# Optimization experiments

Hardware: AMD Instinct MI355X
Metric: run time of the kernel (lower is better)

## Reference

```python
import jax, jax.numpy as jnp
import numpy as np


def _squash(t, axis):
    # matches torch: t / norm * (norm^2 / (1 + norm^2))
    ns = jnp.sum(t * t, axis=axis, keepdims=True)
    norm = jnp.sqrt(ns)
    return t / norm * (ns / (1.0 + ns))


def setup_inputs() -> dict:
    key = jax.random.key(0)
    k1, k2 = jax.random.split(key)
    B, I, A_IN, O, A_OUT = 16, 2048, 16, 64, 32
    x = jax.random.normal(k1, (B, I, A_IN, 1), dtype=jnp.float32)
    # nn.init.normal(std=0.1)
    weights = jax.random.normal(k2, (I, A_IN, O * A_OUT), dtype=jnp.float32) * 0.1
    # nn.init.constant(val=0.1)
    bias = jnp.full((O, A_OUT), 0.1, dtype=jnp.float32)
    return {"x": x, "weights": weights, "bias": bias}


def reference(x, weights, bias):
    B = x.shape[0]
    I, A_IN, OA = weights.shape
    O, A = bias.shape
    NUM_ROUTING = 3  # hardcoded in the torch forward

    # votes = sum over input_atoms of broadcast(x) * weights  -> [B, I, O, A]
    votes = jnp.einsum('bia,iaj->bij', x[..., 0], weights).reshape(B, I, O, A)
    votes_sg = jax.lax.stop_gradient(votes)

    logits = jnp.zeros((B, I, O), dtype=votes.dtype)
    activation = None
    for i in range(NUM_ROUTING):
        route = jax.nn.softmax(logits, axis=2)  # over output_dim
        v = votes if i == NUM_ROUTING - 1 else votes_sg
        # weighted sum over input capsules: [B, O, A]
        preactivate = jnp.einsum('bio,bioa->boa', route, v) + bias
        activation = _squash(preactivate, axis=2)
        if i < NUM_ROUTING - 1:
            # agreement between votes and current output capsules
            distances = jnp.einsum('bioa,boa->bio', votes, activation)
            logits = logits + distances
    return activation
```

## Files before the change

kernel.cpp:

```cpp
#include <hip/hip_runtime.h>
#include <hip/hip_fp16.h>
#include <math.h>

#define B_   16
#define I_   2048
#define AIN_ 16
#define O_   64
#define J_   2048
#define JP_  1024

__device__ __forceinline__ float2 ntload2(const float2* p) {
  union { double d; float2 f; } u;
  u.d = __builtin_nontemporal_load((const double*)p);
  return u.f;
}

__device__ __forceinline__ void unp8(const uint4 u, float2* f) {
  const __half2* h = (const __half2*)&u;
  f[0] = __half22float2(h[0]); f[1] = __half22float2(h[1]);
  f[2] = __half22float2(h[2]); f[3] = __half22float2(h[3]);
}
__device__ __forceinline__ uint4 pk8(float4 a, float4 b) {
  union { uint4 u; __half2 h[4]; } r;
  r.h[0] = __float22half2_rn(make_float2(a.x, a.y));
  r.h[1] = __float22half2_rn(make_float2(a.z, a.w));
  r.h[2] = __float22half2_rn(make_float2(b.x, b.y));
  r.h[3] = __float22half2_rn(make_float2(b.z, b.w));
  return r.u;
}

__global__ __launch_bounds__(256) void votes_p0_kernel(
    const float* __restrict__ x, const float* __restrict__ W,
    __half2* __restrict__ votes, __half2* __restrict__ part0)
{
  __shared__ __half2 x_lds[4][B_][AIN_];
  const int tid = threadIdx.x;
  const int islab = blockIdx.x >> 2, jt = blockIdx.x & 3;
  const int i0 = islab * 4;

  for (int e = tid; e < 4 * B_ * AIN_; e += 256) {
    int il = e >> 8, b = (e >> 4) & 15, a = e & 15;
    float xv = x[((size_t)b * I_ + (i0 + il)) * AIN_ + a];
    x_lds[il][b][a] = __float2half2_rn(xv);
  }
  __syncthreads();

  const int jp = jt * 256 + tid;
  __half2 acc[16];
  #pragma unroll
  for (int b = 0; b < 16; ++b) acc[b] = __float2half2_rn(0.f);

  for (int il = 0; il < 4; ++il) {
    const int i = i0 + il;
    const float2* __restrict__ Wi =
        (const float2*)W + (size_t)i * (AIN_ * JP_) + jp;

    __half2 v[16];
    #pragma unroll
    for (int b = 0; b < 16; ++b) v[b] = __float2half2_rn(0.f);

    #pragma unroll
    for (int a2 = 0; a2 < 8; ++a2) {
      __half2 w0 = __float22half2_rn(ntload2(Wi + (size_t)(2 * a2 + 0) * JP_));
      __half2 w1 = __float22half2_rn(ntload2(Wi + (size_t)(2 * a2 + 1) * JP_));
      #pragma unroll
      for (int b = 0; b < 16; ++b) {
        v[b] = __hfma2(x_lds[il][b][2 * a2],     w0, v[b]);
        v[b] = __hfma2(x_lds[il][b][2 * a2 + 1], w1, v[b]);
      }
    }

    __half2* __restrict__ vo = votes + (size_t)i * (B_ * JP_) + jp;
    #pragma unroll
    for (int b = 0; b < 16; ++b) {
      vo[(size_t)b * JP_] = v[b];
      acc[b] = __hadd2(acc[b], v[b]);
    }
  }

  const __half2 s64 = __float2half2_rn(1.0f / 64.0f);
  __half2* __restrict__ po = part0 + (size_t)blockIdx.x * (B_ * 256) + tid;
  #pragma unroll
  for (int b = 0; b < 16; ++b)
    po[(size_t)b * 256] = __hmul2(acc[b], s64);
}

__global__ __launch_bounds__(256) void reduce_squash0_f16(
    const uint4* __restrict__ part0, const float* __restrict__ bias,
    float* __restrict__ act)
{
  __shared__ float red[64][4][8];
  const int b = blockIdx.x >> 6, o = blockIdx.x & 63;
  const int t = threadIdx.x, s = t >> 2, q = t & 3;
  const uint4* __restrict__ base =
      part0 + (size_t)(o >> 4) * 1024 + b * 64 + (o & 15) * 4 + q;

  float r[8];
  #pragma unroll
  for (int e = 0; e < 8; ++e) r[e] = 0.f;
  #pragma unroll
  for (int k = 0; k < 8; ++k) {
    uint4 u = base[(size_t)(s + 64 * k) * 4096];
    float2 f[4];
    unp8(u, f);
    r[0] += f[0].x; r[1] += f[0].y; r[2] += f[1].x; r[3] += f[1].y;
    r[4] += f[2].x; r[5] += f[2].y; r[6] += f[3].x; r[7] += f[3].y;
  }
  #pragma unroll
  for (int e = 0; e < 8; ++e) red[s][q][e] = r[e];
  __syncthreads();

  if (t < 32) {
    const int q2 = t >> 3, e = t & 7;
    float p = 0.f;
    for (int s2 = 0; s2 < 64; ++s2) p += red[s2][q2][e];
    p += bias[o * 32 + q2 * 8 + e];
    float ns = p * p;
    ns += __shfl_xor(ns, 1);  ns += __shfl_xor(ns, 2);
    ns += __shfl_xor(ns, 4);  ns += __shfl_xor(ns, 8);
    ns += __shfl_xor(ns, 16);
    act[(size_t)b * J_ + o * 32 + q2 * 8 + e] = p * sqrtf(ns) / (1.0f + ns);
  }
}

template<int PASS>
__global__ __launch_bounds__(256) void route_kernel(
    const uint4* __restrict__ votes4, const float* __restrict__ act_in,
    uint4* __restrict__ part, float* __restrict__ logits)
{
  __shared__ float d_lds[128];
  __shared__ float r_lds[128];

  const int t = threadIdx.x;
  const int islab = blockIdx.x >> 3, bq = blockIdx.x & 7;
  const int i0 = islab * 8;
  const int o = t >> 2, l4 = t & 3;
  const float4* __restrict__ actq = (const float4*)act_in;

  float4 av00 = actq[(size_t)(bq * 2 + 0) * 512 + 2 * t];
  float4 av01 = actq[(size_t)(bq * 2 + 0) * 512 + 2 * t + 1];
  float4 av10 = actq[(size_t)(bq * 2 + 1) * 512 + 2 * t];
  float4 av11 = actq[(size_t)(bq * 2 + 1) * 512 + 2 * t + 1];

  float4 ac00 = make_float4(0,0,0,0), ac01 = make_float4(0,0,0,0);
  float4 ac10 = make_float4(0,0,0,0), ac11 = make_float4(0,0,0,0);

  for (int il = 0; il < 8; ++il) {
    const int i = i0 + il;
    float lgv = 0.f;
    if (PASS == 2 && t < 128)
      lgv = logits[((size_t)(bq * 2 + (t >> 6)) * I_ + i) * O_ + (t & 63)];

    const uint4* __restrict__ vo =
        votes4 + (size_t)i * 4096 + (size_t)(bq * 2) * 256 + t;
    float2 f0[4], f1[4];
    unp8(vo[0],   f0);
    unp8(vo[256], f1);

    float c0 = f0[0].x*av00.x + f0[0].y*av00.y + f0[1].x*av00.z + f0[1].y*av00.w
             + f0[2].x*av01.x + f0[2].y*av01.y + f0[3].x*av01.z + f0[3].y*av01.w;
    c0 += __shfl_xor(c0, 1);  c0 += __shfl_xor(c0, 2);
    float c1 = f1[0].x*av10.x + f1[0].y*av10.y + f1[1].x*av10.z + f1[1].y*av10.w
             + f1[2].x*av11.x + f1[2].y*av11.y + f1[3].x*av11.z + f1[3].y*av11.w;
    c1 += __shfl_xor(c1, 1);  c1 += __shfl_xor(c1, 2);
    if (l4 == 0) d_lds[o]      = c0;
    if (l4 == 1) d_lds[64 + o] = c1;
    __syncthreads();

    float ellsave = 0.f;
    if (t < 128) {
      float ell = d_lds[t];
      if (PASS == 2) ell += lgv;
      ellsave = ell;
      float m = ell;
      m = fmaxf(m, __shfl_xor(m, 32)); m = fmaxf(m, __shfl_xor(m, 16));
      m = fmaxf(m, __shfl_xor(m, 8));  m = fmaxf(m, __shfl_xor(m, 4));
      m = fmaxf(m, __shfl_xor(m, 2));  m = fmaxf(m, __shfl_xor(m, 1));
      float e = __expf(ell - m);
      float sd = e;
      sd += __shfl_xor(sd, 32); sd += __shfl_xor(sd, 16); sd += __shfl_xor(sd, 8);
      sd += __shfl_xor(sd, 4);  sd += __shfl_xor(sd, 2);  sd += __shfl_xor(sd, 1);
      r_lds[t] = e / sd;
    }
    __syncthreads();

    if (PASS == 1 && t < 128)
      logits[((size_t)(bq * 2 + (t >> 6)) * I_ + i) * O_ + (t & 63)] = ellsave;

    float r0 = r_lds[o], r1 = r_lds[64 + o];
    ac00.x = fmaf(r0, f0[0].x, ac00.x); ac00.y = fmaf(r0, f0[0].y, ac00.y);
    ac00.z = fmaf(r0, f0[1].x, ac00.z); ac00.w = fmaf(r0, f0[1].y, ac00.w);
    ac01.x = fmaf(r0, f0[2].x, ac01.x); ac01.y = fmaf(r0, f0[2].y, ac01.y);
    ac01.z = fmaf(r0, f0[3].x, ac01.z); ac01.w = fmaf(r0, f0[3].y, ac01.w);
    ac10.x = fmaf(r1, f1[0].x, ac10.x); ac10.y = fmaf(r1, f1[0].y, ac10.y);
    ac10.z = fmaf(r1, f1[1].x, ac10.z); ac10.w = fmaf(r1, f1[1].y, ac10.w);
    ac11.x = fmaf(r1, f1[2].x, ac11.x); ac11.y = fmaf(r1, f1[2].y, ac11.y);
    ac11.z = fmaf(r1, f1[3].x, ac11.z); ac11.w = fmaf(r1, f1[3].y, ac11.w);
  }

  uint4* __restrict__ po =
      part + (size_t)islab * 4096 + (size_t)(bq * 2) * 256 + t;
  po[0]   = pk8(ac00, ac01);
  po[256] = pk8(ac10, ac11);
}

__global__ __launch_bounds__(256) void reduce_squash_f16(
    const uint4* __restrict__ part, const float* __restrict__ bias,
    float* __restrict__ out)
{
  __shared__ float red[64][4][8];
  const int b = blockIdx.x >> 6, o = blockIdx.x & 63;
  const int t = threadIdx.x, s = t >> 2, q = t & 3;
  const uint4* __restrict__ base =
      part + (size_t)b * 256 + o * 4 + q;

  float r[8];
  #pragma unroll
  for (int e = 0; e < 8; ++e) r[e] = 0.f;
  #pragma unroll
  for (int k = 0; k < 4; ++k) {
    uint4 u = base[(size_t)(s + 64 * k) * 4096];
    float2 f[4];
    unp8(u, f);
    r[0] += f[0].x; r[1] += f[0].y; r[2] += f[1].x; r[3] += f[1].y;
    r[4] += f[2].x; r[5] += f[2].y; r[6] += f[3].x; r[7] += f[3].y;
  }
  #pragma unroll
  for (int e = 0; e < 8; ++e) red[s][q][e] = r[e];
  __syncthreads();

  if (t < 32) {
    const int q2 = t >> 3, e = t & 7;
    float p = 0.f;
    for (int s2 = 0; s2 < 64; ++s2) p += red[s2][q2][e];
    p += bias[o * 32 + q2 * 8 + e];
    float ns = p * p;
    ns += __shfl_xor(ns, 1);  ns += __shfl_xor(ns, 2);
    ns += __shfl_xor(ns, 4);  ns += __shfl_xor(ns, 8);
    ns += __shfl_xor(ns, 16);
    out[(size_t)b * J_ + o * 32 + q2 * 8 + e] = p * sqrtf(ns) / (1.0f + ns);
  }
}

__global__ __launch_bounds__(256) void reduce_squash_f32(
    const float* __restrict__ part, const float* __restrict__ bias,
    float* __restrict__ out)
{
  __shared__ float4 red[32][8];
  const int b = blockIdx.x >> 6, o = blockIdx.x & 63;
  const int t = threadIdx.x, s = t >> 3, q = t & 7;
  const float4* __restrict__ base =
      (const float4*)part + (size_t)b * 512 + o * 8 + q;

  float4 acc = make_float4(0.f, 0.f, 0.f, 0.f);
  #pragma unroll
  for (int k = 0; k < 8; ++k) {
    float4 v = base[(size_t)(s + 32 * k) * 8192];
    acc.x += v.x; acc.y += v.y; acc.z += v.z; acc.w += v.w;
  }
  red[s][q] = acc;
  __syncthreads();

  if (t < 8) {
    float4 p = make_float4(0.f, 0.f, 0.f, 0.f);
    for (int s2 = 0; s2 < 32; ++s2) {
      float4 v = red[s2][t];
      p.x += v.x; p.y += v.y; p.z += v.z; p.w += v.w;
    }
    float4 bq4 = ((const float4*)bias)[o * 8 + t];
    p.x += bq4.x; p.y += bq4.y; p.z += bq4.z; p.w += bq4.w;
    float ns = p.x*p.x + p.y*p.y + p.z*p.z + p.w*p.w;
    ns += __shfl_xor(ns, 1);  ns += __shfl_xor(ns, 2);  ns += __shfl_xor(ns, 4);
    float sc = sqrtf(ns) / (1.0f + ns);
    ((float4*)out)[(size_t)b * 512 + o * 8 + t] =
        make_float4(p.x*sc, p.y*sc, p.z*sc, p.w*sc);
  }
}

template<int PASS>
__global__ __launch_bounds__(1024) void fb_pass_kernel(
    const float* __restrict__ x, const float* __restrict__ W,
    const float* __restrict__ act_in, float* __restrict__ part,
    float* __restrict__ logits)
{
  __shared__ float x_lds[8 * B_ * AIN_];
  __shared__ float d_lds[8 * O_];
  __shared__ float r_lds[8 * O_];
  const int tid = threadIdx.x, blk = blockIdx.x, i0 = blk * 8;
  for (int e = tid; e < 8 * B_ * AIN_; e += 1024) {
    int b = e >> 7, il = (e >> 4) & 7, a = e & 15;
    x_lds[il * 256 + b * 16 + a] =
        x[(size_t)b * (I_ * AIN_) + (size_t)(i0 + il) * AIN_ + a];
  }
  __syncthreads();
  const int og = tid >> 4, lg = tid & 15;
  float2 acc[16];
  #pragma unroll
  for (int b = 0; b < 16; ++b) acc[b] = make_float2(0.f, 0.f);
  const float2* __restrict__ Wq   = (const float2*)W;
  const float2* __restrict__ actq = (const float2*)act_in;
  for (int il = 0; il < 8; ++il) {
    const int i = i0 + il;
    const float2* __restrict__ Wi = Wq + (size_t)i * (AIN_ * JP_);
    const float4* __restrict__ xq = (const float4*)x_lds + il * 64;
    for (int h = 0; h < 2; ++h) {
      float2 v[8];
      #pragma unroll
      for (int bb = 0; bb < 8; ++bb) v[bb] = make_float2(0.f, 0.f);
      #pragma unroll
      for (int a4 = 0; a4 < 4; ++a4) {
        float2 w0 = Wi[(size_t)(a4 * 4 + 0) * JP_ + tid];
        float2 w1 = Wi[(size_t)(a4 * 4 + 1) * JP_ + tid];
        float2 w2 = Wi[(size_t)(a4 * 4 + 2) * JP_ + tid];
        float2 w3 = Wi[(size_t)(a4 * 4 + 3) * JP_ + tid];
        #pragma unroll
        for (int bb = 0; bb < 8; ++bb) {
          float4 xv = xq[(h * 8 + bb) * 4 + a4];
          v[bb].x = fmaf(xv.x, w0.x, v[bb].x); v[bb].y = fmaf(xv.x, w0.y, v[bb].y);
          v[bb].x = fmaf(xv.y, w1.x, v[bb].x); v[bb].y = fmaf(xv.y, w1.y, v[bb].y);
          v[bb].x = fmaf(xv.z, w2.x, v[bb].x); v[bb].y = fmaf(xv.z, w2.y, v[bb].y);
          v[bb].x = fmaf(xv.w, w3.x, v[bb].x); v[bb].y = fmaf(xv.w, w3.y, v[bb].y);
        }
      }
      if (PASS == 0) {
        #pragma unroll
        for (int bb = 0; bb < 8; ++bb) {
          acc[h * 8 + bb].x += v[bb].x; acc[h * 8 + bb].y += v[bb].y;
        }
      } else {
        #pragma unroll
        for (int bb = 0; bb < 8; ++bb) {
          const int b = h * 8 + bb;
          float2 avv = actq[(size_t)b * JP_ + tid];
          float c = v[bb].x * avv.x + v[bb].y * avv.y;
          c += __shfl_xor(c, 1); c += __shfl_xor(c, 2);
          c += __shfl_xor(c, 4); c += __shfl_xor(c, 8);
          if (lg == bb) d_lds[bb * 64 + og] = c;
        }
        __syncthreads();
        if (tid < 512) {
          const int bb2 = tid >> 6, o2 = tid & 63;
          const int b2  = h * 8 + bb2;
          float ell = d_lds[tid];
          if (PASS == 2) ell += logits[((size_t)b2 * I_ + i) * O_ + o2];
          if (PASS == 1) logits[((size_t)b2 * I_ + i) * O_ + o2] = ell;
          float m = ell;
          m = fmaxf(m, __shfl_xor(m, 32)); m = fmaxf(m, __shfl_xor(m, 16));
          m = fmaxf(m, __shfl_xor(m, 8));  m = fmaxf(m, __shfl_xor(m, 4));
          m = fmaxf(m, __shfl_xor(m, 2));  m = fmaxf(m, __shfl_xor(m, 1));
          float e = __expf(ell - m);
          float s = e;
          s += __shfl_xor(s, 32); s += __shfl_xor(s, 16); s += __shfl_xor(s, 8);
          s += __shfl_xor(s, 4);  s += __shfl_xor(s, 2);  s += __shfl_xor(s, 1);
          r_lds[tid] = e / s;
        }
        __syncthreads();
        #pragma unroll
        for (int bb = 0; bb < 8; ++bb) {
          float r = r_lds[bb * 64 + og];
          acc[h * 8 + bb].x = fmaf(r, v[bb].x, acc[h * 8 + bb].x);
          acc[h * 8 + bb].y = fmaf(r, v[bb].y, acc[h * 8 + bb].y);
        }
      }
    }
  }
  const float sc = (PASS == 0) ? (1.0f / 64.0f) : 1.0f;
  #pragma unroll
  for (int b = 0; b < 16; ++b) {
    float2* __restrict__ po = (float2*)part +
        (size_t)blk * (B_ * JP_) + (size_t)b * JP_ + tid;
    *po = make_float2(acc[b].x * sc, acc[b].y * sc);
  }
}

extern "C" void kernel_launch(void* const* d_in, const int* in_sizes, int n_in,
                              void* d_out, int out_size, void* d_ws, size_t ws_size,
                              hipStream_t stream) {
  const float* x    = (const float*)d_in[0];
  const float* W    = (const float*)d_in[1];
  const float* bias = (const float*)d_in[2];
  float* out = (float*)d_out;

  float*   part   = (float*)d_ws;
  float*   act    = part + (size_t)256 * (B_ * J_);
  float*   logits = act + (B_ * J_);
  __half2* votes  = (__half2*)(logits + (size_t)B_ * I_ * O_);
  const size_t need = ((size_t)256 * B_ * J_ + B_ * J_ + (size_t)B_ * I_ * O_) * 4
                    + (size_t)I_ * B_ * JP_ * 4;

  if (ws_size >= need) {
    votes_p0_kernel<<<2048, 256, 0, stream>>>(x, W, votes, (__half2*)part);
    reduce_squash0_f16<<<1024, 256, 0, stream>>>((const uint4*)part, bias, act);
    route_kernel<1><<<2048, 256, 0, stream>>>((const uint4*)votes, act,
                                              (uint4*)part, logits);
    reduce_squash_f16<<<1024, 256, 0, stream>>>((const uint4*)part, bias, act);
    route_kernel<2><<<2048, 256, 0, stream>>>((const uint4*)votes, act,
                                              (uint4*)part, logits);
    reduce_squash_f16<<<1024, 256, 0, stream>>>((const uint4*)part, bias, out);
  } else {
    fb_pass_kernel<0><<<256, 1024, 0, stream>>>(x, W, act, part, logits);
    reduce_squash_f32<<<1024, 256, 0, stream>>>(part, bias, act);
    fb_pass_kernel<1><<<256, 1024, 0, stream>>>(x, W, act, part, logits);
    reduce_squash_f32<<<1024, 256, 0, stream>>>(part, bias, act);
    fb_pass_kernel<2><<<256, 1024, 0, stream>>>(x, W, act, part, logits);
    reduce_squash_f32<<<1024, 256, 0, stream>>>(part, bias, out);
  }
}
```

Baseline: 164.6 us.

## Batch routing softmax across eight inputs to cut per-iteration block barriers

```diff
diff --git a/kernel.cpp b/kernel.cpp
--- a/kernel.cpp
+++ b/kernel.cpp
@@ -128,50 +128,51 @@
     const uint4* __restrict__ votes4, const float* __restrict__ act_in,
     uint4* __restrict__ part, float* __restrict__ logits)
 {
-  __shared__ float d_lds[128];
-  __shared__ float r_lds[128];
+  __shared__ float d_lds[8][128];
+  __shared__ float r_lds[8][128];
 
   const int t = threadIdx.x;
   const int islab = blockIdx.x >> 3, bq = blockIdx.x & 7;
   const int i0 = islab * 8;
   const int o = t >> 2, l4 = t & 3;
   const float4* __restrict__ actq = (const float4*)act_in;
-
-  float4 av00 = actq[(size_t)(bq * 2 + 0) * 512 + 2 * t];
-  float4 av01 = actq[(size_t)(bq * 2 + 0) * 512 + 2 * t + 1];
-  float4 av10 = actq[(size_t)(bq * 2 + 1) * 512 + 2 * t];
-  float4 av11 = actq[(size_t)(bq * 2 + 1) * 512 + 2 * t + 1];
-
-  float4 ac00 = make_float4(0,0,0,0), ac01 = make_float4(0,0,0,0);
-  float4 ac10 = make_float4(0,0,0,0), ac11 = make_float4(0,0,0,0);
-
-  for (int il = 0; il < 8; ++il) {
-    const int i = i0 + il;
-    float lgv = 0.f;
-    if (PASS == 2 && t < 128)
-      lgv = logits[((size_t)(bq * 2 + (t >> 6)) * I_ + i) * O_ + (t & 63)];
-
-    const uint4* __restrict__ vo =
-        votes4 + (size_t)i * 4096 + (size_t)(bq * 2) * 256 + t;
-    float2 f0[4], f1[4];
-    unp8(vo[0],   f0);
-    unp8(vo[256], f1);
-
-    float c0 = f0[0].x*av00.x + f0[0].y*av00.y + f0[1].x*av00.z + f0[1].y*av00.w
-             + f0[2].x*av01.x + f0[2].y*av01.y + f0[3].x*av01.z + f0[3].y*av01.w;
-    c0 += __shfl_xor(c0, 1);  c0 += __shfl_xor(c0, 2);
-    float c1 = f1[0].x*av10.x + f1[0].y*av10.y + f1[1].x*av10.z + f1[1].y*av10.w
-             + f1[2].x*av11.x + f1[2].y*av11.y + f1[3].x*av11.z + f1[3].y*av11.w;
-    c1 += __shfl_xor(c1, 1);  c1 += __shfl_xor(c1, 2);
-    if (l4 == 0) d_lds[o]      = c0;
-    if (l4 == 1) d_lds[64 + o] = c1;
-    __syncthreads();
-
-    float ellsave = 0.f;
-    if (t < 128) {
-      float ell = d_lds[t];
-      if (PASS == 2) ell += lgv;
-      ellsave = ell;
+  const uint4* __restrict__ vbase =
+      votes4 + (size_t)i0 * 4096 + (size_t)(bq * 2) * 256 + t;
+
+  {
+    float4 av00 = actq[(size_t)(bq * 2 + 0) * 512 + 2 * t];
+    float4 av01 = actq[(size_t)(bq * 2 + 0) * 512 + 2 * t + 1];
+    float4 av10 = actq[(size_t)(bq * 2 + 1) * 512 + 2 * t];
+    float4 av11 = actq[(size_t)(bq * 2 + 1) * 512 + 2 * t + 1];
+
+    #pragma unroll
+    for (int il = 0; il < 8; ++il) {
+      const uint4* __restrict__ vo = vbase + (size_t)il * 4096;
+      float2 f0[4], f1[4];
+      unp8(vo[0],   f0);
+      unp8(vo[256], f1);
+      float c0 = f0[0].x*av00.x + f0[0].y*av00.y + f0[1].x*av00.z + f0[1].y*av00.w
+               + f0[2].x*av01.x + f0[2].y*av01.y + f0[3].x*av01.z + f0[3].y*av01.w;
+      c0 += __shfl_xor(c0, 1);  c0 += __shfl_xor(c0, 2);
+      float c1 = f1[0].x*av10.x + f1[0].y*av10.y + f1[1].x*av10.z + f1[1].y*av10.w
+               + f1[2].x*av11.x + f1[2].y*av11.y + f1[3].x*av11.z + f1[3].y*av11.w;
+      c1 += __shfl_xor(c1, 1);  c1 += __shfl_xor(c1, 2);
+      if (l4 == 0) d_lds[il][o]      = c0;
+      if (l4 == 1) d_lds[il][64 + o] = c1;
+    }
+  }
+  __syncthreads();
+
+  {
+    const int wv = t >> 6, ln = t & 63;
+    #pragma unroll
+    for (int gg = 0; gg < 4; ++gg) {
+      const int g = wv * 4 + gg;
+      const int il = g >> 1, bb = g & 1;
+      const size_t lix = ((size_t)(bq * 2 + bb) * I_ + (i0 + il)) * O_ + ln;
+      float ell = d_lds[il][bb * 64 + ln];
+      if (PASS == 2) ell += logits[lix];
+      if (PASS == 1) logits[lix] = ell;
       float m = ell;
       m = fmaxf(m, __shfl_xor(m, 32)); m = fmaxf(m, __shfl_xor(m, 16));
       m = fmaxf(m, __shfl_xor(m, 8));  m = fmaxf(m, __shfl_xor(m, 4));
@@ -180,14 +181,20 @@
       float sd = e;
       sd += __shfl_xor(sd, 32); sd += __shfl_xor(sd, 16); sd += __shfl_xor(sd, 8);
       sd += __shfl_xor(sd, 4);  sd += __shfl_xor(sd, 2);  sd += __shfl_xor(sd, 1);
-      r_lds[t] = e / sd;
-    }
-    __syncthreads();
-
-    if (PASS == 1 && t < 128)
-      logits[((size_t)(bq * 2 + (t >> 6)) * I_ + i) * O_ + (t & 63)] = ellsave;
-
-    float r0 = r_lds[o], r1 = r_lds[64 + o];
+      r_lds[il][bb * 64 + ln] = e / sd;
+    }
+  }
+  __syncthreads();
+
+  float4 ac00 = make_float4(0,0,0,0), ac01 = make_float4(0,0,0,0);
+  float4 ac10 = make_float4(0,0,0,0), ac11 = make_float4(0,0,0,0);
+  #pragma unroll
+  for (int il = 0; il < 8; ++il) {
+    const uint4* __restrict__ vo = vbase + (size_t)il * 4096;
+    float2 f0[4], f1[4];
+    unp8(vo[0],   f0);
+    unp8(vo[256], f1);
+    float r0 = r_lds[il][o], r1 = r_lds[il][64 + o];
     ac00.x = fmaf(r0, f0[0].x, ac00.x); ac00.y = fmaf(r0, f0[0].y, ac00.y);
     ac00.z = fmaf(r0, f0[1].x, ac00.z); ac00.w = fmaf(r0, f0[1].y, ac00.w);
     ac01.x = fmaf(r0, f0[2].x, ac01.x); ac01.y = fmaf(r0, f0[2].y, ac01.y);
```

After: 189.5 us. 1.15x slower.

## Fuse routing passes into one cooperative kernel with grid-wide syncs

Applied to the files above, without the earlier changes.

```diff
diff --git a/kernel.cpp b/kernel.cpp
--- a/kernel.cpp
+++ b/kernel.cpp
@@ -1,4 +1,5 @@
 #include <hip/hip_runtime.h>
+#include <hip/hip_cooperative_groups.h>
 #include <hip/hip_fp16.h>
 #include <math.h>
 
@@ -8,6 +9,8 @@
 #define O_   64
 #define J_   2048
 #define JP_  1024
+
+namespace cg = cooperative_groups;
 
 __device__ __forceinline__ float2 ntload2(const float2* p) {
   union { double d; float2 f; } u;
@@ -85,12 +88,11 @@
     po[(size_t)b * 256] = __hmul2(acc[b], s64);
 }
 
-__global__ __launch_bounds__(256) void reduce_squash0_f16(
-    const uint4* __restrict__ part0, const float* __restrict__ bias,
-    float* __restrict__ act)
-{
-  __shared__ float red[64][4][8];
-  const int b = blockIdx.x >> 6, o = blockIdx.x & 63;
+__device__ __forceinline__ void reduce0_body(
+    int bid, const uint4* __restrict__ part0, const float* __restrict__ bias,
+    float* __restrict__ act, float* smem)
+{
+  const int b = bid >> 6, o = bid & 63;
   const int t = threadIdx.x, s = t >> 2, q = t & 3;
   const uint4* __restrict__ base =
       part0 + (size_t)(o >> 4) * 1024 + b * 64 + (o & 15) * 4 + q;
@@ -107,13 +109,13 @@
     r[4] += f[2].x; r[5] += f[2].y; r[6] += f[3].x; r[7] += f[3].y;
   }
   #pragma unroll
-  for (int e = 0; e < 8; ++e) red[s][q][e] = r[e];
+  for (int e = 0; e < 8; ++e) smem[(s * 4 + q) * 8 + e] = r[e];
   __syncthreads();
 
   if (t < 32) {
     const int q2 = t >> 3, e = t & 7;
     float p = 0.f;
-    for (int s2 = 0; s2 < 64; ++s2) p += red[s2][q2][e];
+    for (int s2 = 0; s2 < 64; ++s2) p += smem[(s2 * 4 + q2) * 8 + e];
     p += bias[o * 32 + q2 * 8 + e];
     float ns = p * p;
     ns += __shfl_xor(ns, 1);  ns += __shfl_xor(ns, 2);
@@ -123,16 +125,51 @@
   }
 }
 
+__device__ __forceinline__ void reduce_body(
+    int bid, const uint4* __restrict__ part, const float* __restrict__ bias,
+    float* __restrict__ dst, float* smem)
+{
+  const int b = bid >> 6, o = bid & 63;
+  const int t = threadIdx.x, s = t >> 2, q = t & 3;
+  const uint4* __restrict__ base = part + (size_t)b * 256 + o * 4 + q;
+
+  float r[8];
+  #pragma unroll
+  for (int e = 0; e < 8; ++e) r[e] = 0.f;
+  #pragma unroll
+  for (int k = 0; k < 4; ++k) {
+    uint4 u = base[(size_t)(s + 64 * k) * 4096];
+    float2 f[4];
+    unp8(u, f);
+    r[0] += f[0].x; r[1] += f[0].y; r[2] += f[1].x; r[3] += f[1].y;
+    r[4] += f[2].x; r[5] += f[2].y; r[6] += f[3].x; r[7] += f[3].y;
+  }
+  #pragma unroll
+  for (int e = 0; e < 8; ++e) smem[(s * 4 + q) * 8 + e] = r[e];
+  __syncthreads();
+
+  if (t < 32) {
+    const int q2 = t >> 3, e = t & 7;
+    float p = 0.f;
+    for (int s2 = 0; s2 < 64; ++s2) p += smem[(s2 * 4 + q2) * 8 + e];
+    p += bias[o * 32 + q2 * 8 + e];
+    float ns = p * p;
+    ns += __shfl_xor(ns, 1);  ns += __shfl_xor(ns, 2);
+    ns += __shfl_xor(ns, 4);  ns += __shfl_xor(ns, 8);
+    ns += __shfl_xor(ns, 16);
+    dst[(size_t)b * J_ + o * 32 + q2 * 8 + e] = p * sqrtf(ns) / (1.0f + ns);
+  }
+}
+
 template<int PASS>
-__global__ __launch_bounds__(256) void route_kernel(
-    const uint4* __restrict__ votes4, const float* __restrict__ act_in,
-    uint4* __restrict__ part, float* __restrict__ logits)
-{
-  __shared__ float d_lds[128];
-  __shared__ float r_lds[128];
-
+__device__ __forceinline__ void route_body(
+    int sb, const uint4* __restrict__ votes4, const float* __restrict__ act_in,
+    uint4* __restrict__ part, float* __restrict__ logits, float* smem)
+{
+  float* d_lds = smem;
+  float* r_lds = smem + 128;
   const int t = threadIdx.x;
-  const int islab = blockIdx.x >> 3, bq = blockIdx.x & 7;
+  const int islab = sb >> 3, bq = sb & 7;
   const int i0 = islab * 8;
   const int o = t >> 2, l4 = t & 3;
   const float4* __restrict__ actq = (const float4*)act_in;
@@ -204,42 +241,52 @@
   po[256] = pk8(ac10, ac11);
 }
 
+__global__ __launch_bounds__(256, 4) void routing_mega(
+    const uint4* __restrict__ votes4, uint4* __restrict__ part,
+    const float* __restrict__ bias, float* __restrict__ act,
+    float* __restrict__ logits, float* __restrict__ out)
+{
+  __shared__ float smem[2048];
+  cg::grid_group grid = cg::this_grid();
+
+  reduce0_body(blockIdx.x, part, bias, act, smem);
+  grid.sync();
+  route_body<1>(blockIdx.x * 2 + 0, votes4, act, part, logits, smem);
+  __syncthreads();
+  route_body<1>(blockIdx.x * 2 + 1, votes4, act, part, logits, smem);
+  grid.sync();
+  reduce_body(blockIdx.x, part, bias, act, smem);
+  grid.sync();
+  route_body<2>(blockIdx.x * 2 + 0, votes4, act, part, logits, smem);
+  __syncthreads();
+  route_body<2>(blockIdx.x * 2 + 1, votes4, act, part, logits, smem);
+  grid.sync();
+  reduce_body(blockIdx.x, part, bias, out, smem);
+}
+
+__global__ __launch_bounds__(256) void reduce_squash0_f16(
+    const uint4* __restrict__ part0, const float* __restrict__ bias,
+    float* __restrict__ act)
+{
+  __shared__ float smem[2048];
+  reduce0_body(blockIdx.x, part0, bias, act, smem);
+}
+
+template<int PASS>
+__global__ __launch_bounds__(256) void route_kernel(
+    const uint4* __restrict__ votes4, const float* __restrict__ act_in,
+    uint4* __restrict__ part, float* __restrict__ logits)
+{
+  __shared__ float smem[256];
+  route_body<PASS>(blockIdx.x, votes4, act_in, part, logits, smem);
+}
+
 __global__ __launch_bounds__(256) void reduce_squash_f16(
     const uint4* __restrict__ part, const float* __restrict__ bias,
     float* __restrict__ out)
 {
-  __shared__ float red[64][4][8];
-  const int b = blockIdx.x >> 6, o = blockIdx.x & 63;
-  const int t = threadIdx.x, s = t >> 2, q = t & 3;
-  const uint4* __restrict__ base =
-      part + (size_t)b * 256 + o * 4 + q;
-
-  float r[8];
-  #pragma unroll
-  for (int e = 0; e < 8; ++e) r[e] = 0.f;
-  #pragma unroll
-  for (int k = 0; k < 4; ++k) {
-    uint4 u = base[(size_t)(s + 64 * k) * 4096];
-    float2 f[4];
-    unp8(u, f);
-    r[0] += f[0].x; r[1] += f[0].y; r[2] += f[1].x; r[3] += f[1].y;
-    r[4] += f[2].x; r[5] += f[2].y; r[6] += f[3].x; r[7] += f[3].y;
-  }
-  #pragma unroll
-  for (int e = 0; e < 8; ++e) red[s][q][e] = r[e];
-  __syncthreads();
-
-  if (t < 32) {
-    const int q2 = t >> 3, e = t & 7;
-    float p = 0.f;
-    for (int s2 = 0; s2 < 64; ++s2) p += red[s2][q2][e];
-    p += bias[o * 32 + q2 * 8 + e];
-    float ns = p * p;
-    ns += __shfl_xor(ns, 1);  ns += __shfl_xor(ns, 2);
-    ns += __shfl_xor(ns, 4);  ns += __shfl_xor(ns, 8);
-    ns += __shfl_xor(ns, 16);
-    out[(size_t)b * J_ + o * 32 + q2 * 8 + e] = p * sqrtf(ns) / (1.0f + ns);
-  }
+  __shared__ float smem[2048];
+  reduce_body(blockIdx.x, part, bias, out, smem);
 }
 
 __global__ __launch_bounds__(256) void reduce_squash_f32(
@@ -390,6 +437,28 @@
 
   if (ws_size >= need) {
     votes_p0_kernel<<<2048, 256, 0, stream>>>(x, W, votes, (__half2*)part);
+
+    int coop = 0;
+    int dev = 0;
+    (void)hipGetDevice(&dev);
+    (void)hipDeviceGetAttribute(&coop, hipDeviceAttributeCooperativeLaunch, dev);
+
+    if (coop) {
+      const uint4* votes4p = (const uint4*)votes;
+      uint4*       partp   = (uint4*)part;
+      const float* biasp   = bias;
+      float*       actp    = act;
+      float*       logitsp = logits;
+      float*       outp    = out;
+      void* args[] = { (void*)&votes4p, (void*)&partp, (void*)&biasp,
+                       (void*)&actp, (void*)&logitsp, (void*)&outp };
+      hipError_t e = hipLaunchCooperativeKernel(
+          reinterpret_cast<void*>(&routing_mega),
+          dim3(1024), dim3(256), args, 0, stream);
+      if (e == hipSuccess) return;
+      (void)hipGetLastError();
+    }
+
     reduce_squash0_f16<<<1024, 256, 0, stream>>>((const uint4*)part, bias, act);
     route_kernel<1><<<2048, 256, 0, stream>>>((const uint4*)votes, act,
                                               (uint4*)part, logits);
```

Result: slower. 589.0 us (+257.8%).
